# Optimization experiments

Hardware: AMD Instinct MI355X
Metric: run time of the kernel (lower is better)

## Reference

```python
import jax, jax.numpy as jnp
import numpy as np

EPS = 1e-7  # keras backend epsilon used inside K.ctc_decode's log


def setup_inputs() -> dict:
    key = jax.random.key(0)
    B, T, C = 64, 256, 2500
    logits = jax.random.normal(key, (B, T, C), dtype=jnp.float32)
    # K.ctc_decode expects softmax probabilities as input
    inputs = jax.nn.softmax(logits, axis=-1)
    return {"inputs": inputs}


def reference(inputs):
    """CTC best-path decode (beam_width=1), matching K.ctc_decode semantics:
    - log(probs + eps)
    - per-frame argmax, merge consecutive repeats, remove blank (= C-1)
    - dense output padded with -1, shape [B, T]
    - score = -(sum over frames of max log-prob), shape [B, 1]
    """
    B, T, C = inputs.shape
    blank = C - 1
    logp = jnp.log(inputs + EPS)                      # [B, T, C]
    best = jnp.argmax(logp, axis=-1)                  # [B, T] int
    max_lp = jnp.max(logp, axis=-1)                   # [B, T]

    # collapse: drop tokens equal to previous frame's token, then drop blanks
    prev = jnp.concatenate(
        [jnp.full((B, 1), -1, dtype=best.dtype), best[:, :-1]], axis=1
    )
    keep = (best != blank) & (best != prev)           # [B, T] bool

    # left-compact kept tokens into a -1 padded buffer (extra trash column T)
    pos = jnp.cumsum(keep.astype(jnp.int32), axis=1) - 1   # [B, T]
    pos = jnp.where(keep, pos, T)
    out = jnp.full((B, T + 1), -1, dtype=jnp.int32)
    batch_idx = jnp.arange(B)[:, None]
    out = out.at[batch_idx, pos].set(best.astype(jnp.int32))
    decoded = out[:, :T]                              # [B, T], -1 padded

    scores = -jnp.sum(max_lp, axis=1, keepdims=True)  # [B, 1]
    return decoded, scores
```

## Files before the change

kernel.cpp:

```cpp
#include <hip/hip_runtime.h>
#include <math.h>

#define BATCH 64
#define TLEN  256
#define NCLS  2500
#define BLANK (NCLS - 1)
#define EPSF  1e-7f

__global__ __launch_bounds__(256) void ctc_rowmax_kernel(
    const float* __restrict__ in, int* __restrict__ best, float* __restrict__ maxlp) {
  const int row = blockIdx.x;
  const float4* p4 = (const float4*)(in + (size_t)row * NCLS);
  const int tid = threadIdx.x;

  float vmax = -1.0f;
  int   vidx = 0;

  for (int i = tid; i < NCLS / 4; i += 256) {
    float4 v = p4[i];
    int base = i << 2;
    if (v.x > vmax || (v.x == vmax && base     < vidx)) { vmax = v.x; vidx = base;     }
    if (v.y > vmax || (v.y == vmax && base + 1 < vidx)) { vmax = v.y; vidx = base + 1; }
    if (v.z > vmax || (v.z == vmax && base + 2 < vidx)) { vmax = v.z; vidx = base + 2; }
    if (v.w > vmax || (v.w == vmax && base + 3 < vidx)) { vmax = v.w; vidx = base + 3; }
  }

  for (int off = 32; off > 0; off >>= 1) {
    float ov = __shfl_down(vmax, off);
    int   oi = __shfl_down(vidx, off);
    if (ov > vmax || (ov == vmax && oi < vidx)) { vmax = ov; vidx = oi; }
  }

  __shared__ float s_v[4];
  __shared__ int   s_i[4];
  const int wid = tid >> 6, lane = tid & 63;
  if (lane == 0) { s_v[wid] = vmax; s_i[wid] = vidx; }
  __syncthreads();
  if (tid == 0) {
    for (int w = 1; w < 4; ++w) {
      if (s_v[w] > vmax || (s_v[w] == vmax && s_i[w] < vidx)) { vmax = s_v[w]; vidx = s_i[w]; }
    }
    best[row]  = vidx;
    maxlp[row] = logf(vmax + EPSF);
  }
}

__global__ __launch_bounds__(256) void ctc_decode_kernel(
    const int* __restrict__ best, const float* __restrict__ maxlp,
    float* __restrict__ dec, float* __restrict__ score) {
  const int b = blockIdx.x, t = threadIdx.x;

  __shared__ int s_best[TLEN];
  __shared__ int s_scan[TLEN];

  const int my = best[b * TLEN + t];
  s_best[t] = my;
  __syncthreads();

  const int prev = (t == 0) ? -1 : s_best[t - 1];
  const int keep = (my != BLANK && my != prev) ? 1 : 0;

  s_scan[t] = keep;
  __syncthreads();
  for (int off = 1; off < TLEN; off <<= 1) {
    int add = (t >= off) ? s_scan[t - off] : 0;
    __syncthreads();
    s_scan[t] += add;
    __syncthreads();
  }
  const int pos = s_scan[t] - 1;

  dec[b * TLEN + t] = -1.0f;
  __syncthreads();
  if (keep) dec[b * TLEN + pos] = (float)my;

  float v = maxlp[b * TLEN + t];
  for (int off = 32; off > 0; off >>= 1) v += __shfl_down(v, off);
  __shared__ float s_sum[4];
  if ((t & 63) == 0) s_sum[t >> 6] = v;
  __syncthreads();
  if (t == 0) {
    float s = s_sum[0] + s_sum[1] + s_sum[2] + s_sum[3];
    score[b] = -s;
  }
}

extern "C" void kernel_launch(void* const* d_in, const int* in_sizes, int n_in,
                              void* d_out, int out_size, void* d_ws, size_t ws_size,
                              hipStream_t stream) {
  const float* in = (const float*)d_in[0];
  float* out = (float*)d_out;
  int*   best  = (int*)d_ws;
  float* maxlp = (float*)((char*)d_ws + (size_t)BATCH * TLEN * sizeof(int));

  ctc_rowmax_kernel<<<BATCH * TLEN, 256, 0, stream>>>(in, best, maxlp);
  ctc_decode_kernel<<<BATCH, 256, 0, stream>>>(best, maxlp, out, out + BATCH * TLEN);
}
```

Baseline: 35.20 us.

## Assign one wavefront per row and use wave-level scan in decode

```diff
diff --git a/kernel.cpp b/kernel.cpp
--- a/kernel.cpp
+++ b/kernel.cpp
@@ -6,23 +6,39 @@
 #define NCLS  2500
 #define BLANK (NCLS - 1)
 #define EPSF  1e-7f
+#define NF4   (NCLS / 4)
+#define FULL_IT 9
+#define TAIL_LANES (NF4 - FULL_IT * 64)
 
 __global__ __launch_bounds__(256) void ctc_rowmax_kernel(
     const float* __restrict__ in, int* __restrict__ best, float* __restrict__ maxlp) {
-  const int row = blockIdx.x;
-  const float4* p4 = (const float4*)(in + (size_t)row * NCLS);
-  const int tid = threadIdx.x;
+  const int wid  = threadIdx.x >> 6;
+  const int lane = threadIdx.x & 63;
+  const int row  = (blockIdx.x << 2) + wid;
+  const float4* __restrict__ p4 = (const float4*)(in + (size_t)row * NCLS) + lane;
+
+  float4 v[FULL_IT + 1];
+  #pragma unroll
+  for (int it = 0; it < FULL_IT; ++it) v[it] = p4[it << 6];
+  const bool tail = lane < TAIL_LANES;
+  if (tail) v[FULL_IT] = p4[FULL_IT << 6];
 
   float vmax = -1.0f;
   int   vidx = 0;
-
-  for (int i = tid; i < NCLS / 4; i += 256) {
-    float4 v = p4[i];
-    int base = i << 2;
-    if (v.x > vmax || (v.x == vmax && base     < vidx)) { vmax = v.x; vidx = base;     }
-    if (v.y > vmax || (v.y == vmax && base + 1 < vidx)) { vmax = v.y; vidx = base + 1; }
-    if (v.z > vmax || (v.z == vmax && base + 2 < vidx)) { vmax = v.z; vidx = base + 2; }
-    if (v.w > vmax || (v.w == vmax && base + 3 < vidx)) { vmax = v.w; vidx = base + 3; }
+  #pragma unroll
+  for (int it = 0; it < FULL_IT; ++it) {
+    const int base = (it << 8) + (lane << 2);
+    if (v[it].x > vmax) { vmax = v[it].x; vidx = base;     }
+    if (v[it].y > vmax) { vmax = v[it].y; vidx = base + 1; }
+    if (v[it].z > vmax) { vmax = v[it].z; vidx = base + 2; }
+    if (v[it].w > vmax) { vmax = v[it].w; vidx = base + 3; }
+  }
+  if (tail) {
+    const int base = (FULL_IT << 8) + (lane << 2);
+    if (v[FULL_IT].x > vmax) { vmax = v[FULL_IT].x; vidx = base;     }
+    if (v[FULL_IT].y > vmax) { vmax = v[FULL_IT].y; vidx = base + 1; }
+    if (v[FULL_IT].z > vmax) { vmax = v[FULL_IT].z; vidx = base + 2; }
+    if (v[FULL_IT].w > vmax) { vmax = v[FULL_IT].w; vidx = base + 3; }
   }
 
   for (int off = 32; off > 0; off >>= 1) {
@@ -30,16 +46,7 @@
     int   oi = __shfl_down(vidx, off);
     if (ov > vmax || (ov == vmax && oi < vidx)) { vmax = ov; vidx = oi; }
   }
-
-  __shared__ float s_v[4];
-  __shared__ int   s_i[4];
-  const int wid = tid >> 6, lane = tid & 63;
-  if (lane == 0) { s_v[wid] = vmax; s_i[wid] = vidx; }
-  __syncthreads();
-  if (tid == 0) {
-    for (int w = 1; w < 4; ++w) {
-      if (s_v[w] > vmax || (s_v[w] == vmax && s_i[w] < vidx)) { vmax = s_v[w]; vidx = s_i[w]; }
-    }
+  if (lane == 0) {
     best[row]  = vidx;
     maxlp[row] = logf(vmax + EPSF);
   }
@@ -49,40 +56,38 @@
     const int* __restrict__ best, const float* __restrict__ maxlp,
     float* __restrict__ dec, float* __restrict__ score) {
   const int b = blockIdx.x, t = threadIdx.x;
+  const int lane = t & 63, wid = t >> 6;
 
-  __shared__ int s_best[TLEN];
-  __shared__ int s_scan[TLEN];
+  const int my   = best[b * TLEN + t];
+  const int prev = (t == 0) ? -1 : best[b * TLEN + t - 1];
+  const int keep = (my != BLANK && my != prev) ? 1 : 0;
 
-  const int my = best[b * TLEN + t];
-  s_best[t] = my;
+  int x = keep;
+  #pragma unroll
+  for (int off = 1; off < 64; off <<= 1) {
+    int y = __shfl_up(x, off);
+    if (lane >= off) x += y;
+  }
+  __shared__ int   s_wsum[4];
+  __shared__ float s_fsum[4];
+  if (lane == 63) s_wsum[wid] = x;
+
+  float v = maxlp[b * TLEN + t];
+  #pragma unroll
+  for (int off = 32; off > 0; off >>= 1) v += __shfl_down(v, off);
+  if (lane == 0) s_fsum[wid] = v;
   __syncthreads();
 
-  const int prev = (t == 0) ? -1 : s_best[t - 1];
-  const int keep = (my != BLANK && my != prev) ? 1 : 0;
-
-  s_scan[t] = keep;
-  __syncthreads();
-  for (int off = 1; off < TLEN; off <<= 1) {
-    int add = (t >= off) ? s_scan[t - off] : 0;
-    __syncthreads();
-    s_scan[t] += add;
-    __syncthreads();
-  }
-  const int pos = s_scan[t] - 1;
+  int offset = 0;
+  #pragma unroll
+  for (int w = 0; w < 4; ++w) offset += (w < wid) ? s_wsum[w] : 0;
+  const int pos = offset + x - 1;
 
   dec[b * TLEN + t] = -1.0f;
   __syncthreads();
   if (keep) dec[b * TLEN + pos] = (float)my;
 
-  float v = maxlp[b * TLEN + t];
-  for (int off = 32; off > 0; off >>= 1) v += __shfl_down(v, off);
-  __shared__ float s_sum[4];
-  if ((t & 63) == 0) s_sum[t >> 6] = v;
-  __syncthreads();
-  if (t == 0) {
-    float s = s_sum[0] + s_sum[1] + s_sum[2] + s_sum[3];
-    score[b] = -s;
-  }
+  if (t == 0) score[b] = -(s_fsum[0] + s_fsum[1] + s_fsum[2] + s_fsum[3]);
 }
 
 extern "C" void kernel_launch(void* const* d_in, const int* in_sizes, int n_in,
@@ -93,6 +98,6 @@
   int*   best  = (int*)d_ws;
   float* maxlp = (float*)((char*)d_ws + (size_t)BATCH * TLEN * sizeof(int));
 
-  ctc_rowmax_kernel<<<BATCH * TLEN, 256, 0, stream>>>(in, best, maxlp);
+  ctc_rowmax_kernel<<<(BATCH * TLEN) / 4, 256, 0, stream>>>(in, best, maxlp);
   ctc_decode_kernel<<<BATCH, 256, 0, stream>>>(best, maxlp, out, out + BATCH * TLEN);
 }
```

Result: faster. 32.48 us (-7.7%).
